# Performance work log

Measured on AMD Instinct MI355X. Metric: run time of the kernel, lower is better.

## Reference

```python
import jax, jax.numpy as jnp
import numpy as np
from jax import lax

FILTERS = [(1, 32), (2, 32), (3, 64), (4, 128), (5, 256), (6, 512), (7, 1024)]
CHAR_VOCAB, CHAR_DIM, MAX_CHARS = 262, 16, 50
N_FILTERS = sum(n for _, n in FILTERS)  # 2048
PROJ_DIM = 512
B, S = 16, 256


def setup_inputs() -> dict:
    key = jax.random.key(0)
    ks = jax.random.split(key, 32)
    inp = {}
    inp["words"] = jax.random.randint(ks[0], (B, S), 0, 50000)
    inp["chars"] = jax.random.randint(ks[1], (B, S, MAX_CHARS), 0, CHAR_VOCAB)
    inp["char_emb"] = jax.random.normal(ks[2], (CHAR_VOCAB, CHAR_DIM), jnp.float32) * 0.1
    for i, (w, n) in enumerate(FILTERS):
        inp[f"conv_w_{i}"] = jax.random.normal(ks[3 + i], (n, CHAR_DIM, w), jnp.float32) * 0.1
        inp[f"conv_b_{i}"] = jnp.zeros((n,), jnp.float32)
    for j in range(2):
        inp[f"hw_w_{j}"] = jax.random.normal(ks[12 + j], (2 * N_FILTERS, N_FILTERS), jnp.float32) * 0.02
        # Highway init: transform bias = 0, gate bias = 1
        inp[f"hw_b_{j}"] = jnp.concatenate([jnp.zeros((N_FILTERS,), jnp.float32), jnp.ones((N_FILTERS,), jnp.float32)])
    inp["proj_w"] = jax.random.normal(ks[20], (PROJ_DIM, N_FILTERS), jnp.float32) * 0.02
    inp["proj_b"] = jnp.zeros((PROJ_DIM,), jnp.float32)
    return inp


def _char_cnn(chars, char_emb, conv_ws, conv_bs, hw_ws, hw_bs, proj_w, proj_b):
    b, s, L = chars.shape
    # (B*S, CHAR_DIM, L)
    x = char_emb[chars].reshape(b * s, L, -1).transpose(0, 2, 1)
    convs = []
    for w, bias in zip(conv_ws, conv_bs):
        # Conv1d valid, NCW layout; y: (N, num, L-width+1)
        y = lax.conv_general_dilated(x, w, (1,), "VALID", dimension_numbers=("NCH", "OIH", "NCH"))
        y = y + bias[None, :, None]
        y = jnp.max(y, axis=-1)          # max over time
        convs.append(jax.nn.relu(y))      # activation
    h = jnp.concatenate(convs, axis=-1)   # (N, 2048)
    d = h.shape[-1]
    for W, bb in zip(hw_ws, hw_bs):
        p = h @ W.T + bb
        nonlinear = jax.nn.relu(p[:, :d])
        gate = jax.nn.sigmoid(p[:, d:])
        h = gate * h + (1.0 - gate) * nonlinear
    out = h @ proj_w.T + proj_b
    return out.reshape(b, s, -1)


def reference(words, chars, char_emb,
              conv_w_0, conv_b_0, conv_w_1, conv_b_1, conv_w_2, conv_b_2,
              conv_w_3, conv_b_3, conv_w_4, conv_b_4, conv_w_5, conv_b_5,
              conv_w_6, conv_b_6, hw_w_0, hw_b_0, hw_w_1, hw_b_1, proj_w, proj_b):
    conv_ws = [conv_w_0, conv_w_1, conv_w_2, conv_w_3, conv_w_4, conv_w_5, conv_w_6]
    conv_bs = [conv_b_0, conv_b_1, conv_b_2, conv_b_3, conv_b_4, conv_b_5, conv_b_6]
    return _char_cnn(chars, char_emb, conv_ws, conv_bs, [hw_w_0, hw_w_1], [hw_b_0, hw_b_1], proj_w, proj_b)
```

## Files before the change

### kernel.cpp

```cpp
#include <hip/hip_runtime.h>
#include <hip/hip_bf16.h>


#define NTOK 4096
#define NF   2048
#define KDIM 2048
#define HID  4096
#define PDIM 512

typedef __attribute__((ext_vector_type(4))) float floatx4;
typedef __attribute__((ext_vector_type(8))) short shortx8;

__device__ inline void async_copy16(const void* g, void* l) {
  __builtin_amdgcn_global_load_lds(
      (const __attribute__((address_space(1))) void*)(uintptr_t)g,
      (__attribute__((address_space(3))) void*)(uint32_t)(uintptr_t)l,
      16, 0, 0);
}

__global__ __launch_bounds__(256) void cvt_kernel(
    const float* __restrict__ s, __hip_bfloat16* __restrict__ d, int n) {
  int i = blockIdx.x * 256 + threadIdx.x;
  if (i < n) d[i] = __float2bfloat16(s[i]);
}

__global__ __launch_bounds__(256) void cvt_hw(
    const float* __restrict__ s, __hip_bfloat16* __restrict__ d) {
  int i = blockIdx.x * 256 + threadIdx.x;
  int r = i >> 11, k = i & 2047;
  int sr = (r >> 1) + (r & 1) * 2048;
  d[i] = __float2bfloat16(s[(size_t)sr * 2048 + k]);
}

__global__ __launch_bounds__(256) void conv_wprep(
    const float* __restrict__ w0, const float* __restrict__ w1,
    const float* __restrict__ w2, const float* __restrict__ w3,
    const float* __restrict__ w4, const float* __restrict__ w5,
    const float* __restrict__ w6,
    const float* __restrict__ b0, const float* __restrict__ b1,
    const float* __restrict__ b2, const float* __restrict__ b3,
    const float* __restrict__ b4, const float* __restrict__ b5,
    const float* __restrict__ b6, const float* __restrict__ emb,
    __hip_bfloat16* __restrict__ Wb, float* __restrict__ Bc,
    __hip_bfloat16* __restrict__ embb) {
  int idx = blockIdx.x * 256 + threadIdx.x;
  const int start[7] = {0, 32, 64, 128, 256, 512, 1024};
  const float* ws[7] = {w0, w1, w2, w3, w4, w5, w6};
  const float* bs[7] = {b0, b1, b2, b3, b4, b5, b6};
  if (idx < 262144) {
    int ch = idx >> 7, kp = idx & 127;
    int f = (ch >= 32) + (ch >= 64) + (ch >= 128) + (ch >= 256) +
            (ch >= 512) + (ch >= 1024);
    int w = f + 1, lc = ch - start[f];
    int d = kp & 15, k = kp >> 4;
    float v = (k < w) ? ws[f][((size_t)lc * 16 + d) * w + k] : 0.f;
    Wb[idx] = __float2bfloat16(v);
  } else if (idx < 262144 + 2048) {
    int ch = idx - 262144;
    int f = (ch >= 32) + (ch >= 64) + (ch >= 128) + (ch >= 256) +
            (ch >= 512) + (ch >= 1024);
    Bc[ch] = bs[f][ch - start[f]];
  } else if (idx < 262144 + 2048 + 4192) {
    int e = idx - 262144 - 2048;
    embb[e] = __float2bfloat16(emb[e]);
  }
}

template <int NKT, int NT, int ROWS>
__global__ __launch_bounds__(256) void conv_k(
    const int* __restrict__ chars, const __hip_bfloat16* __restrict__ embb,
    const __hip_bfloat16* __restrict__ Wb, const float* __restrict__ bias,
    __hip_bfloat16* __restrict__ h, int chbase) {
  __shared__ __align__(16) __hip_bfloat16 Xs[2 * 4 * ROWS * 24];
  int tid = threadIdx.x, wave = tid >> 6, lane = tid & 63;
  int frow = lane & 15, q = lane >> 4;
  int chb = chbase + blockIdx.y * 64;
  int tokbase = blockIdx.x * 32;

  shortx8 wreg[NKT][4];
#pragma unroll
  for (int kt = 0; kt < NKT; ++kt)
#pragma unroll
    for (int j = 0; j < 4; ++j)
      wreg[kt][j] = *(const shortx8*)(
          Wb + (size_t)(chb + j * 16 + frow) * 128 + kt * 32 + q * 8);

  float blane = bias[chb + lane];
  int Tvj[4];
#pragma unroll
  for (int j = 0; j < 4; ++j) {
    int ch = chb + j * 16 + frow;
    int w = 1 + (ch >= 32) + (ch >= 64) + (ch >= 128) + (ch >= 256) +
            (ch >= 512) + (ch >= 1024);
    Tvj[j] = 51 - w;
  }

  auto stage = [&](int g, int buf) {
    constexpr int NST = 4 * ROWS;
#pragma unroll
    for (int rep = 0; rep < (NST + 255) / 256; ++rep) {
      int rr = tid + rep * 256;
      if (rr < NST) {
        int tk = rr / ROWS, r = rr - tk * ROWS;
        __hip_bfloat16* dst = Xs + ((size_t)(buf * 4 + tk) * ROWS + r) * 24;
        if (r < 50) {
          int c = chars[(size_t)(tokbase + g * 4 + tk) * 50 + r];
          const shortx8* e = (const shortx8*)(embb + c * 16);
          *(shortx8*)(dst) = e[0];
          *(shortx8*)(dst + 8) = e[1];
        } else if (g <= 1) {
          shortx8 z = {0, 0, 0, 0, 0, 0, 0, 0};
          *(shortx8*)(dst) = z;
          *(shortx8*)(dst + 8) = z;
        }
      }
    }
  };

  stage(0, 0);
  __syncthreads();

  const floatx4 zero = {0.f, 0.f, 0.f, 0.f};
#pragma unroll 1
  for (int g = 0; g < 8; ++g) {
    if (g < 7) stage(g + 1, (g + 1) & 1);

    const __hip_bfloat16* Xw = Xs + (size_t)((g & 1) * 4 + wave) * ROWS * 24;
    floatx4 acc[NT][4];

#pragma unroll
    for (int kt = 0; kt < NKT; ++kt) {
      int kk = kt * 2 + (q >> 1);
      int d0 = (q & 1) * 8;
      shortx8 xf[NT];
#pragma unroll
      for (int i = 0; i < NT; ++i)
        xf[i] = *(const shortx8*)(Xw + (i * 16 + frow + kk) * 24 + d0);
#pragma unroll
      for (int i = 0; i < NT; ++i)
#pragma unroll
        for (int j = 0; j < 4; ++j) {
          if (kt == 0)
            acc[i][j] = __builtin_amdgcn_mfma_f32_16x16x32_bf16(
                xf[i], wreg[0][j], zero, 0, 0, 0);
          else
            acc[i][j] = __builtin_amdgcn_mfma_f32_16x16x32_bf16(
                xf[i], wreg[kt][j], acc[i][j], 0, 0, 0);
        }
    }

    float vj[4];
#pragma unroll
    for (int j = 0; j < 4; ++j) {
      float v = -1e30f;
#pragma unroll
      for (int i = 0; i < NT; ++i) {
#pragma unroll
        for (int r = 0; r < 4; ++r) {
          if (i < 2) {
            v = fmaxf(v, acc[i][j][r]);
          } else {
            int t = i * 16 + q * 4 + r;
            if (t < Tvj[j]) v = fmaxf(v, acc[i][j][r]);
          }
        }
      }
      v = fmaxf(v, __shfl_xor(v, 16));
      v = fmaxf(v, __shfl_xor(v, 32));
      vj[j] = v;
    }
    float r0 = (q & 2) ? vj[2] : vj[0];
    float r1 = (q & 2) ? vj[3] : vj[1];
    float rv = (q & 1) ? r1 : r0;
    int tok = tokbase + g * 4 + wave;
    h[(size_t)tok * NF + chb + lane] =
        __float2bfloat16(fmaxf(rv + blane, 0.f));
    __syncthreads();
  }
}

__global__ __launch_bounds__(256) void gemm_hw(
    const __hip_bfloat16* __restrict__ A, const __hip_bfloat16* __restrict__ B,
    const float* __restrict__ hwb, __hip_bfloat16* __restrict__ Hdst) {
  const int K = KDIM;
  __shared__ __align__(16) __hip_bfloat16 As[128 * 64];
  __shared__ __align__(16) __hip_bfloat16 Bs[128 * 64];
  int tid = threadIdx.x;
  int wave = tid >> 6, lane = tid & 63;
  int wr = wave >> 1, wc = wave & 1;
  int bn = blockIdx.y, bm = blockIdx.x;

  int sr8 = lane >> 3;
  int sc8 = lane & 7;
  int frow = lane & 15;
  int q    = lane >> 4;

  floatx4 acc[4][4];
  floatx4 zero = {0.f, 0.f, 0.f, 0.f};
#pragma unroll
  for (int i = 0; i < 4; ++i)
#pragma unroll
    for (int j = 0; j < 4; ++j) acc[i][j] = zero;

  const __hip_bfloat16* Ab = A + (size_t)bn * 128 * K;
  const __hip_bfloat16* Bb = B + (size_t)bm * 128 * K;

  for (int kb = 0; kb < K; kb += 64) {
    __syncthreads();
#pragma unroll
    for (int it = 0; it < 4; ++it) {
      int seg = wave * 4 + it;
      int r = seg * 8 + sr8;
      int gc = sc8 ^ (r & 7);
      async_copy16(Ab + (size_t)r * K + kb + gc * 8, (char*)As + seg * 1024);
      async_copy16(Bb + (size_t)r * K + kb + gc * 8, (char*)Bs + seg * 1024);
    }
    __syncthreads();

#pragma unroll
    for (int s = 0; s < 2; ++s) {
      shortx8 af[4], bf[4];
#pragma unroll
      for (int i = 0; i < 4; ++i) {
        int r = wr * 64 + i * 16 + frow;
        af[i] = *(const shortx8*)(As + r * 64 + ((s * 4 + q) ^ (r & 7)) * 8);
      }
#pragma unroll
      for (int j = 0; j < 4; ++j) {
        int r = wc * 64 + j * 16 + frow;
        bf[j] = *(const shortx8*)(Bs + r * 64 + ((s * 4 + q) ^ (r & 7)) * 8);
      }
#pragma unroll
      for (int i = 0; i < 4; ++i)
#pragma unroll
        for (int j = 0; j < 4; ++j)
          acc[i][j] = __builtin_amdgcn_mfma_f32_16x16x32_bf16(
              af[i], bf[j], acc[i][j], 0, 0, 0);
    }
  }

  int crow0 = bn * 128 + wr * 64 + q * 4;
  int ccol0 = bm * 128 + wc * 64 + frow;
#pragma unroll
  for (int i = 0; i < 4; ++i)
#pragma unroll
    for (int j = 0; j < 4; ++j) {
      int gcol = ccol0 + j * 16;
      float bb = (gcol & 1) ? hwb[2048 + (gcol >> 1)] : hwb[gcol >> 1];
#pragma unroll
      for (int r = 0; r < 4; ++r) {
        int row = crow0 + i * 16 + r;
        float v = acc[i][j][r] + bb;
        float partner = __shfl_xor(v, 1);
        if (!(lane & 1)) {
          float gte = 1.f / (1.f + expf(-partner));
          int ch = gcol >> 1;
          float hold = __bfloat162float(A[(size_t)row * 2048 + ch]);
          float hnew = gte * hold + (1.f - gte) * fmaxf(v, 0.f);
          Hdst[(size_t)row * 2048 + ch] = __float2bfloat16(hnew);
        }
      }
    }
}

__global__ __launch_bounds__(256) void gemm_proj(
    const __hip_bfloat16* __restrict__ A, const __hip_bfloat16* __restrict__ B,
    float* __restrict__ C, const float* __restrict__ bias) {
  const int K = KDIM;
  __shared__ __align__(16) __hip_bfloat16 As[32 * 64];
  __shared__ __align__(16) __hip_bfloat16 Bs[128 * 64];
  int tid = threadIdx.x;
  int wave = tid >> 6, lane = tid & 63;
  int wr = wave >> 1, wc = wave & 1;
  int bn = blockIdx.y, bm = blockIdx.x;

  int sr8 = lane >> 3, sc8 = lane & 7;
  int frow = lane & 15, q = lane >> 4;

  floatx4 acc[4];
  floatx4 zero = {0.f, 0.f, 0.f, 0.f};
#pragma unroll
  for (int j = 0; j < 4; ++j) acc[j] = zero;

  const __hip_bfloat16* Ab = A + (size_t)bn * 32 * K;
  const __hip_bfloat16* Bb = B + (size_t)bm * 128 * K;

  for (int kb = 0; kb < K; kb += 64) {
    __syncthreads();
    {
      int r = wave * 8 + sr8;
      int gc = sc8 ^ (r & 7);
      async_copy16(Ab + (size_t)r * K + kb + gc * 8, (char*)As + wave * 1024);
    }
#pragma unroll
    for (int it = 0; it < 4; ++it) {
      int seg = wave * 4 + it;
      int r = seg * 8 + sr8;
      int gc = sc8 ^ (r & 7);
      async_copy16(Bb + (size_t)r * K + kb + gc * 8, (char*)Bs + seg * 1024);
    }
    __syncthreads();

#pragma unroll
    for (int s = 0; s < 2; ++s) {
      shortx8 af, bf[4];
      {
        int r = wr * 16 + frow;
        af = *(const shortx8*)(As + r * 64 + ((s * 4 + q) ^ (r & 7)) * 8);
      }
#pragma unroll
      for (int j = 0; j < 4; ++j) {
        int r = wc * 64 + j * 16 + frow;
        bf[j] = *(const shortx8*)(Bs + r * 64 + ((s * 4 + q) ^ (r & 7)) * 8);
      }
#pragma unroll
      for (int j = 0; j < 4; ++j)
        acc[j] = __builtin_amdgcn_mfma_f32_16x16x32_bf16(af, bf[j], acc[j],
                                                          0, 0, 0);
    }
  }

  int crow0 = bn * 32 + wr * 16 + q * 4;
  int ccol0 = bm * 128 + wc * 64 + frow;
#pragma unroll
  for (int j = 0; j < 4; ++j) {
    int c = ccol0 + j * 16;
#pragma unroll
    for (int r = 0; r < 4; ++r) {
      int row = crow0 + r;
      C[(size_t)row * PDIM + c] = acc[j][r] + bias[c];
    }
  }
}

extern "C" void kernel_launch(void* const* d_in, const int* in_sizes, int n_in,
                              void* d_out, int out_size, void* d_ws, size_t ws_size,
                              hipStream_t stream) {
  const int*   chars  = (const int*)d_in[1];
  const float* emb    = (const float*)d_in[2];
  const float* cw[7];
  const float* cb[7];
  for (int i = 0; i < 7; ++i) {
    cw[i] = (const float*)d_in[3 + 2 * i];
    cb[i] = (const float*)d_in[4 + 2 * i];
  }
  const float* hw_w0  = (const float*)d_in[17];
  const float* hw_b0  = (const float*)d_in[18];
  const float* hw_w1  = (const float*)d_in[19];
  const float* hw_b1  = (const float*)d_in[20];
  const float* proj_w = (const float*)d_in[21];
  const float* proj_b = (const float*)d_in[22];
  float* out = (float*)d_out;

  char* ws = (char*)d_ws;
  __hip_bfloat16* h      = (__hip_bfloat16*)(ws);
  __hip_bfloat16* h2     = (__hip_bfloat16*)(ws + (16ull << 20));
  __hip_bfloat16* convWb = (__hip_bfloat16*)(ws + (32ull << 20));
  float*          convBc = (float*)(ws + (32ull << 20) + 524288);
  __hip_bfloat16* embb   = (__hip_bfloat16*)(ws + (32ull << 20) + 524288 + 8192);
  __hip_bfloat16* w0b    = (__hip_bfloat16*)(ws + (48ull << 20));
  __hip_bfloat16* w1b    = (__hip_bfloat16*)(ws + (64ull << 20));
  __hip_bfloat16* pwb    = (__hip_bfloat16*)(ws + (80ull << 20));

  cvt_hw<<<(HID * KDIM) / 256, 256, 0, stream>>>(hw_w0, w0b);
  cvt_hw<<<(HID * KDIM) / 256, 256, 0, stream>>>(hw_w1, w1b);
  cvt_kernel<<<(PDIM * KDIM) / 256, 256, 0, stream>>>(proj_w, pwb, PDIM * KDIM);
  conv_wprep<<<(262144 + 2048 + 4192 + 255) / 256, 256, 0, stream>>>(
      cw[0], cw[1], cw[2], cw[3], cw[4], cw[5], cw[6],
      cb[0], cb[1], cb[2], cb[3], cb[4], cb[5], cb[6], emb,
      convWb, convBc, embb);

  conv_k<1, 4, 72><<<dim3(128, 1), 256, 0, stream>>>(chars, embb, convWb,
                                                     convBc, h, 0);
  conv_k<2, 3, 56><<<dim3(128, 3), 256, 0, stream>>>(chars, embb, convWb,
                                                     convBc, h, 64);
  conv_k<3, 3, 56><<<dim3(128, 12), 256, 0, stream>>>(chars, embb, convWb,
                                                      convBc, h, 256);
  conv_k<4, 3, 56><<<dim3(128, 16), 256, 0, stream>>>(chars, embb, convWb,
                                                      convBc, h, 1024);

  gemm_hw<<<dim3(HID / 128, NTOK / 128), 256, 0, stream>>>(h, w0b, hw_b0, h2);
  gemm_hw<<<dim3(HID / 128, NTOK / 128), 256, 0, stream>>>(h2, w1b, hw_b1, h);
  gemm_proj<<<dim3(PDIM / 128, NTOK / 32), 256, 0, stream>>>(h, pwb, out,
                                                             proj_b);
}
```

Baseline: 522.1 us.

## Rewrite highway GEMM as 256x256 double-buffered 8-wave kernel with interleaved prefetch

Replaces the 128x128, 4-wave highway GEMM with a 256x256 tile, 8-wave (512-thread) kernel. It double-buffers LDS and interleaves async global-to-LDS prefetch of the next K tile with MFMA phases, and adds an XCD-aware block swizzle and s_setprio around the MFMA bursts. The aim is higher arithmetic intensity per byte loaded and hiding load latency behind compute, in place of the serial load-sync-compute loop. The cost is 128 KB of LDS per block, far more accumulator registers, and 256 blocks, which may limit occupancy.

```diff
diff --git a/kernel.cpp b/kernel.cpp
--- a/kernel.cpp
+++ b/kernel.cpp
@@ -16,6 +16,12 @@
       (const __attribute__((address_space(1))) void*)(uintptr_t)g,
       (__attribute__((address_space(3))) void*)(uint32_t)(uintptr_t)l,
       16, 0, 0);
+}
+
+__device__ inline void block_barrier() {
+  asm volatile("" ::: "memory");
+  __builtin_amdgcn_s_barrier();
+  asm volatile("" ::: "memory");
 }
 
 __global__ __launch_bounds__(256) void cvt_kernel(
@@ -179,70 +185,137 @@
   }
 }
 
-__global__ __launch_bounds__(256) void gemm_hw(
+__global__ __launch_bounds__(512, 2) void gemm_hw8(
     const __hip_bfloat16* __restrict__ A, const __hip_bfloat16* __restrict__ B,
     const float* __restrict__ hwb, __hip_bfloat16* __restrict__ Hdst) {
-  const int K = KDIM;
-  __shared__ __align__(16) __hip_bfloat16 As[128 * 64];
-  __shared__ __align__(16) __hip_bfloat16 Bs[128 * 64];
+  __shared__ __align__(16) __hip_bfloat16 As[2 * 256 * 64];
+  __shared__ __align__(16) __hip_bfloat16 Bs[2 * 256 * 64];
   int tid = threadIdx.x;
   int wave = tid >> 6, lane = tid & 63;
-  int wr = wave >> 1, wc = wave & 1;
-  int bn = blockIdx.y, bm = blockIdx.x;
-
-  int sr8 = lane >> 3;
-  int sc8 = lane & 7;
-  int frow = lane & 15;
-  int q    = lane >> 4;
-
-  floatx4 acc[4][4];
-  floatx4 zero = {0.f, 0.f, 0.f, 0.f};
-#pragma unroll
-  for (int i = 0; i < 4; ++i)
+  int wr = wave >> 2, wc = wave & 3;
+  int sr8 = lane >> 3, sc8 = lane & 7;
+  int frow = lane & 15, q = lane >> 4;
+
+  int wg = blockIdx.x;
+  int swz = (wg & 7) * 32 + (wg >> 3);
+  int bm = swz & 15;
+  int bn = swz >> 4;
+
+  const __hip_bfloat16* Ab = A + (size_t)bn * 256 * KDIM;
+  const __hip_bfloat16* Bb = B + (size_t)bm * 256 * KDIM;
+
+  floatx4 acc[8][4];
+  const floatx4 zero = {0.f, 0.f, 0.f, 0.f};
+#pragma unroll
+  for (int i = 0; i < 8; ++i)
 #pragma unroll
     for (int j = 0; j < 4; ++j) acc[i][j] = zero;
 
-  const __hip_bfloat16* Ab = A + (size_t)bn * 128 * K;
-  const __hip_bfloat16* Bb = B + (size_t)bm * 128 * K;
-
-  for (int kb = 0; kb < K; kb += 64) {
-    __syncthreads();
-#pragma unroll
-    for (int it = 0; it < 4; ++it) {
-      int seg = wave * 4 + it;
-      int r = seg * 8 + sr8;
-      int gc = sc8 ^ (r & 7);
-      async_copy16(Ab + (size_t)r * K + kb + gc * 8, (char*)As + seg * 1024);
-      async_copy16(Bb + (size_t)r * K + kb + gc * 8, (char*)Bs + seg * 1024);
-    }
-    __syncthreads();
-
-#pragma unroll
-    for (int s = 0; s < 2; ++s) {
-      shortx8 af[4], bf[4];
-#pragma unroll
-      for (int i = 0; i < 4; ++i) {
-        int r = wr * 64 + i * 16 + frow;
-        af[i] = *(const shortx8*)(As + r * 64 + ((s * 4 + q) ^ (r & 7)) * 8);
-      }
-#pragma unroll
-      for (int j = 0; j < 4; ++j) {
-        int r = wc * 64 + j * 16 + frow;
-        bf[j] = *(const shortx8*)(Bs + r * 64 + ((s * 4 + q) ^ (r & 7)) * 8);
-      }
-#pragma unroll
-      for (int i = 0; i < 4; ++i)
-#pragma unroll
-        for (int j = 0; j < 4; ++j)
-          acc[i][j] = __builtin_amdgcn_mfma_f32_16x16x32_bf16(
-              af[i], bf[j], acc[i][j], 0, 0, 0);
-    }
-  }
-
-  int crow0 = bn * 128 + wr * 64 + q * 4;
-  int ccol0 = bm * 128 + wc * 64 + frow;
-#pragma unroll
-  for (int i = 0; i < 4; ++i)
+  auto stage_half = [&](const __hip_bfloat16* gsrc, __hip_bfloat16* lbase,
+                        int d, int hf, int kb) {
+#pragma unroll
+    for (int it = 0; it < 2; ++it) {
+      int row = hf * 128 + (wave * 2 + it) * 8;
+      int r = row + sr8;
+      int gc = sc8 ^ sr8;
+      async_copy16(gsrc + (size_t)r * KDIM + kb + gc * 8,
+                   (char*)lbase + ((size_t)d * 256 + row) * 128);
+    }
+  };
+
+  shortx8 b_[4][2];
+  shortx8 aA[2][2];
+
+#define LDA(Asd, i0)                                                         \
+  {                                                                          \
+    _Pragma("unroll") for (int ii = 0; ii < 2; ++ii) {                       \
+      _Pragma("unroll") for (int s = 0; s < 2; ++s) {                        \
+        int r = wr * 128 + ((i0) + ii) * 16 + frow;                          \
+        aA[ii][s] = *(const shortx8*)((Asd) + r * 64 +                       \
+                                      (((s * 4 + q) ^ (frow & 7)) << 3));    \
+      }                                                                      \
+    }                                                                        \
+  }
+
+#define LDB(Bsd)                                                             \
+  {                                                                          \
+    _Pragma("unroll") for (int j = 0; j < 4; ++j) {                          \
+      _Pragma("unroll") for (int s = 0; s < 2; ++s) {                        \
+        int r = wc * 64 + j * 16 + frow;                                     \
+        b_[j][s] = *(const shortx8*)((Bsd) + r * 64 +                        \
+                                     (((s * 4 + q) ^ (frow & 7)) << 3));     \
+      }                                                                      \
+    }                                                                        \
+  }
+
+#define MMA2(i0)                                                             \
+  {                                                                          \
+    __builtin_amdgcn_s_setprio(1);                                           \
+    _Pragma("unroll") for (int s = 0; s < 2; ++s) {                          \
+      _Pragma("unroll") for (int ii = 0; ii < 2; ++ii) {                     \
+        _Pragma("unroll") for (int j = 0; j < 4; ++j) {                      \
+          acc[(i0) + ii][j] = __builtin_amdgcn_mfma_f32_16x16x32_bf16(       \
+              aA[ii][s], b_[j][s], acc[(i0) + ii][j], 0, 0, 0);              \
+        }                                                                    \
+      }                                                                      \
+    }                                                                        \
+    __builtin_amdgcn_s_setprio(0);                                           \
+  }
+
+  stage_half(Bb, Bs, 0, 0, 0);
+  stage_half(Bb, Bs, 0, 1, 0);
+  stage_half(Ab, As, 0, 0, 0);
+  stage_half(Ab, As, 0, 1, 0);
+  stage_half(Bb, Bs, 1, 0, 64);
+  asm volatile("s_waitcnt vmcnt(2)" ::: "memory");
+  block_barrier();
+
+  const int NTILE = KDIM / 64;
+#pragma unroll 2
+  for (int T = 0; T < NTILE; ++T) {
+    int d = T & 1, d1 = d ^ 1;
+    const __hip_bfloat16* Asd = As + d * 16384;
+    const __hip_bfloat16* Bsd = Bs + d * 16384;
+    int kn = (T + 1) * 64;
+
+    LDA(Asd, 0);
+    LDB(Bsd);
+    if (T + 1 < NTILE) stage_half(Bb, Bs, d1, 1, kn);
+    block_barrier();
+    MMA2(0);
+    block_barrier();
+
+    LDA(Asd, 2);
+    if (T + 1 < NTILE) stage_half(Ab, As, d1, 0, kn);
+    block_barrier();
+    MMA2(2);
+    block_barrier();
+
+    LDA(Asd, 4);
+    if (T + 1 < NTILE) stage_half(Ab, As, d1, 1, kn);
+    block_barrier();
+    MMA2(4);
+    block_barrier();
+
+    LDA(Asd, 6);
+    if (T + 2 < NTILE) stage_half(Bb, Bs, d, 0, kn + 64);
+    block_barrier();
+    MMA2(6);
+    if (T + 2 < NTILE) {
+      asm volatile("s_waitcnt vmcnt(2)" ::: "memory");
+    } else if (T + 1 < NTILE) {
+      asm volatile("s_waitcnt vmcnt(0)" ::: "memory");
+    }
+    block_barrier();
+  }
+#undef LDA
+#undef LDB
+#undef MMA2
+
+  int crow0 = bn * 256 + wr * 128 + q * 4;
+  int ccol0 = bm * 256 + wc * 64 + frow;
+#pragma unroll
+  for (int i = 0; i < 8; ++i)
 #pragma unroll
     for (int j = 0; j < 4; ++j) {
       int gcol = ccol0 + j * 16;
@@ -379,8 +452,8 @@
   conv_k<4, 3, 56><<<dim3(128, 16), 256, 0, stream>>>(chars, embb, convWb,
                                                       convBc, h, 1024);
 
-  gemm_hw<<<dim3(HID / 128, NTOK / 128), 256, 0, stream>>>(h, w0b, hw_b0, h2);
-  gemm_hw<<<dim3(HID / 128, NTOK / 128), 256, 0, stream>>>(h2, w1b, hw_b1, h);
+  gemm_hw8<<<dim3(256), 512, 0, stream>>>(h, w0b, hw_b0, h2);
+  gemm_hw8<<<dim3(256), 512, 0, stream>>>(h2, w1b, hw_b1, h);
   gemm_proj<<<dim3(PDIM / 128, NTOK / 32), 256, 0, stream>>>(h, pwb, out,
                                                              proj_b);
 }
```

New measurement: 469.3 us. -10.1%, faster.
